# Performance work log

Hardware: AMD Instinct MI355X
Metric: run time of the kernel (lower is better)

The kernel has to match this reference:

```python
import jax, jax.numpy as jnp
import numpy as np

BN_EPS = 1e-5

def setup_inputs() -> dict:
    key = jax.random.key(0)
    ks = jax.random.split(key, 13)
    bs, ch, hei, wei = 4, 32, 32, 128  # n_features = wei = 128, ch = n_features//4
    nf = wei
    def p(k, shape, s=0.05):
        return jax.random.normal(k, shape, dtype=jnp.float32) * s
    return {
        "head": jax.random.normal(ks[0], (bs, ch, hei, wei), dtype=jnp.float32),
        "tail": jax.random.normal(ks[1], (bs, ch, hei, wei), dtype=jnp.float32),
        "R_q": p(ks[2], (nf, nf)), "R_k": p(ks[3], (nf, nf)),
        "R_v": p(ks[4], (nf, nf)), "R_W": p(ks[5], (nf, nf)),
        "F_q": p(ks[6], (nf, nf)), "F_k": p(ks[7], (nf, nf)),
        "F_v": p(ks[8], (nf, nf)), "F_W": p(ks[9], (nf, nf)),
        "conv_w": p(ks[10], (2, 2 * ch, 1, 1)),
        "conv_b": jnp.zeros((2,), jnp.float32),
        "bn_w": jnp.ones((2,), jnp.float32),
        "bn_b": jnp.zeros((2,), jnp.float32),
        "bn_mean": jnp.zeros((2,), jnp.float32),
        "bn_var": jnp.ones((2,), jnp.float32),
        "flag": 1,
    }

def _affinity(head, tail, conv_w, conv_b, bn_w, bn_b, bn_mean, bn_var):
    # 1x1 conv -> eval-mode BatchNorm2d -> ReLU -> softmax over channel dim
    x = jnp.concatenate([head, tail], axis=1)                       # [b,2c,h,w]
    a = jnp.einsum('bchw,oc->bohw', x, conv_w[:, :, 0, 0]) + conv_b[None, :, None, None]
    scale = (bn_w / jnp.sqrt(bn_var + BN_EPS))[None, :, None, None]
    a = (a - bn_mean[None, :, None, None]) * scale + bn_b[None, :, None, None]
    a = jax.nn.relu(a)
    return jax.nn.softmax(a, axis=1)                                # torch legacy dim=1 for 4D

def reference(head, tail, R_q, R_k, R_v, R_W, F_q, F_k, F_v, F_W,
              conv_w, conv_b, bn_w, bn_b, bn_mean, bn_var, flag):
    bs, ch, hei, wei = head.shape
    L = hei * wei
    ic = ch  # inter_channels == ch by construction
    aff = _affinity(head, tail, conv_w, conv_b, bn_w, bn_b, bn_mean, bn_var)
    if flag:
        alpha = aff[:, 0].reshape(bs, L, 1)                          # broadcast over last axis
        q = (head @ R_q).reshape(bs, ic, L).transpose(0, 2, 1)       # [b,L,ic]
        t_k = (tail @ F_k).reshape(bs, ic, L).transpose(0, 2, 1)     # [b,L,ic]
        t_v = (tail @ F_v).reshape(bs, ic, L)                        # [b,ic,L]
        f_t = t_k @ t_v                                              # [b,L,L]
        h_k = (head @ R_k).reshape(bs, ic, L).transpose(0, 2, 1)
        h_v = (head @ R_v).reshape(bs, ic, L)
        f_h = h_k @ h_v                                              # [b,L,L]
        att = jax.nn.softmax(alpha * f_t + f_h, axis=-1)
        y = (att @ q).transpose(0, 2, 1).reshape(bs, ic, hei, wei)
        return y @ R_W + head
    else:
        alpha = aff[:, 1].reshape(bs, L, 1)
        q = (tail @ F_q).reshape(bs, ic, L).transpose(0, 2, 1)
        h_k = (head @ R_k).reshape(bs, ic, L).transpose(0, 2, 1)
        h_v = (head @ R_v).reshape(bs, ic, L)
        f_h = h_k @ h_v
        t_k = (tail @ F_k).reshape(bs, ic, L).transpose(0, 2, 1)
        t_v = (tail @ F_v).reshape(bs, ic, L)
        f_t = t_k @ t_v
        att = jax.nn.softmax(alpha * f_h + f_t, axis=-1)
        y = (att @ q).transpose(0, 2, 1).reshape(bs, ic, hei, wei)
        return y @ F_W + tail
```

## Files before the change

kernel.cpp:

```cpp
#include <hip/hip_runtime.h>
#include <hip/hip_bf16.h>
#include <stdint.h>

typedef unsigned short u16;
typedef unsigned int u32;
typedef __attribute__((ext_vector_type(8))) short short8;
typedef __attribute__((ext_vector_type(4))) short short4_t;
typedef __attribute__((ext_vector_type(4))) float f32x4;
typedef __attribute__((ext_vector_type(16))) float f32x16;

#define MFMA16(A,B,C) __builtin_amdgcn_mfma_f32_16x16x32_bf16((A),(B),(C),0,0,0)
#define MFMA32(A,B,C) __builtin_amdgcn_mfma_f32_32x32x16_bf16((A),(B),(C),0,0,0)
#define L2E 1.4426950408889634f

__device__ __forceinline__ u16 f2bf(float f) {
  u32 x = __float_as_uint(f);
  u32 r = x + 0x7fffu + ((x >> 16) & 1u);
  return (u16)(r >> 16);
}
__device__ __forceinline__ float bf2f(short v) {
  return __uint_as_float((u32)(u16)v << 16);
}
__device__ __forceinline__ u32 pack_bf2(float a, float b) {
  __hip_bfloat162 h = __float22bfloat162_rn(make_float2(a, b));
  u32 u; __builtin_memcpy(&u, &h, 4); return u;
}
__device__ __forceinline__ short8 mk_frag(u32 w0, u32 w1, u32 w2, u32 w3) {
  union { u32 u[4]; short8 s; } cv;
  cv.u[0] = w0; cv.u[1] = w1; cv.u[2] = w2; cv.u[3] = w3;
  return cv.s;
}

#if __has_builtin(__builtin_amdgcn_permlane32_swap)
__device__ __forceinline__ float half_max(float x) {
  u32 xu = __float_as_uint(x);
  auto a = __builtin_amdgcn_permlane32_swap(xu, xu, false, false);
  return fmaxf(__uint_as_float(a[0]), __uint_as_float(a[1]));
}
__device__ __forceinline__ float half_sum(float x) {
  u32 xu = __float_as_uint(x);
  auto a = __builtin_amdgcn_permlane32_swap(xu, xu, false, false);
  return __uint_as_float(a[0]) + __uint_as_float(a[1]);
}
#else
__device__ __forceinline__ float half_max(float x) {
  return fmaxf(x, __shfl_xor(x, 32, 64));
}
__device__ __forceinline__ float half_sum(float x) {
  return x + __shfl_xor(x, 32, 64);
}
#endif

__global__ void kprep(const float* R_q, const float* R_k, const float* R_v,
                      const float* R_W, const float* F_q, const float* F_k,
                      const float* F_v, const float* F_W, const int* flagp,
                      u16* matT)
{
  int flag = *flagp;
  const float* S;
  int m = blockIdx.x;
  if (flag) {
    const float* s[6] = {R_q, R_k, R_v, F_k, F_v, R_W}; S = s[m];
  } else {
    const float* s[6] = {F_q, F_k, F_v, R_k, R_v, F_W}; S = s[m];
  }
  u16* dst = matT + m * 16384;
  int base = blockIdx.y * 2048;
  for (int idx = base + threadIdx.x; idx < base + 2048; idx += blockDim.x) {
    int k = idx >> 7, n = idx & 127;
    dst[n * 128 + k] = f2bf(S[idx]);
  }
}

__global__ __launch_bounds__(256) void kproj(const float* __restrict__ head,
    const float* __restrict__ tail, const u16* __restrict__ matT,
    const float* __restrict__ conv_w, const float* __restrict__ conv_b,
    const float* __restrict__ bn_w, const float* __restrict__ bn_b,
    const float* __restrict__ bn_mean, const float* __restrict__ bn_var,
    u16* __restrict__ qT, u16* __restrict__ KQ,
    u16* __restrict__ Vc, const int* __restrict__ flagp)
{
  __shared__ u16 lds_t[128][34];
  __shared__ float s_alpha[128];
  const int flag = *flagp;
  const float* X1 = flag ? head : tail;
  const float* X2 = flag ? tail : head;
  const int bh = blockIdx.x, g = blockIdx.y;
  const int b = bh >> 5, h = bh & 31;
  const float* src = (g < 3) ? X1 : X2;
  const u16* Bm = matT + g * 16384;
  const int tid = threadIdx.x, lane = tid & 63, wid = tid >> 6;
  const int lrow = lane & 15, lg = lane >> 4;
  const int rt = wid & 1, cbase = (wid >> 1) * 64;

  if (g == 3) {
    if (tid < 128) {
      int w = tid;
      const float* hp = head + ((size_t)b * 1024 + h) * 128 + w;
      const float* tp = tail + ((size_t)b * 1024 + h) * 128 + w;
      float a0 = 0.f, a1 = 0.f;
      for (int c = 0; c < 32; ++c) {
        float xh = hp[c * 4096];
        float xt = tp[c * 4096];
        a0 += xh * conv_w[c]      + xt * conv_w[32 + c];
        a1 += xh * conv_w[64 + c] + xt * conv_w[96 + c];
      }
      const float eps = 1e-5f;
      a0 += conv_b[0]; a1 += conv_b[1];
      a0 = (a0 - bn_mean[0]) * (bn_w[0] * rsqrtf(bn_var[0] + eps)) + bn_b[0];
      a1 = (a1 - bn_mean[1]) * (bn_w[1] * rsqrtf(bn_var[1] + eps)) + bn_b[1];
      a0 = fmaxf(a0, 0.f); a1 = fmaxf(a1, 0.f);
      float asel = flag ? a0 : a1, aoth = flag ? a1 : a0;
      s_alpha[w] = 1.f / (1.f + __expf(aoth - asel));
    }
    __syncthreads();
  }

  f32x4 acc[4] = {};
  const float* Arow = src + (((size_t)b * 32 + rt * 16 + lrow) * 32 + h) * 128;
  #pragma unroll
  for (int k0 = 0; k0 < 128; k0 += 32) {
    const float* ap = Arow + k0 + lg * 8;
    float4 f0 = *reinterpret_cast<const float4*>(ap);
    float4 f1 = *reinterpret_cast<const float4*>(ap + 4);
    short8 af = mk_frag(pack_bf2(f0.x, f0.y), pack_bf2(f0.z, f0.w),
                        pack_bf2(f1.x, f1.y), pack_bf2(f1.z, f1.w));
    #pragma unroll
    for (int cc = 0; cc < 4; ++cc) {
      short8 bf = *reinterpret_cast<const short8*>(
          Bm + (cbase + cc * 16 + lrow) * 128 + k0 + lg * 8);
      acc[cc] = MFMA16(af, bf, acc[cc]);
    }
  }
  #pragma unroll
  for (int cc = 0; cc < 4; ++cc) {
    int n = cbase + cc * 16 + lrow;
    float asc = (g == 1) ? L2E : 1.f;
    if (g == 3) asc = s_alpha[n] * L2E;
    #pragma unroll
    for (int rr = 0; rr < 4; ++rr) {
      int c = rt * 16 + lg * 4 + rr;
      lds_t[n][c] = f2bf(acc[cc][rr] * asc);
    }
  }
  __syncthreads();
  if (g == 0) {
    int c = tid >> 3, w0 = (tid & 7) * 16;
    int tw[8];
    #pragma unroll
    for (int i2 = 0; i2 < 8; ++i2)
      tw[i2] = (int)lds_t[w0 + 2 * i2][c] | ((int)lds_t[w0 + 2 * i2 + 1][c] << 16);
    int4* dst = reinterpret_cast<int4*>(qT + ((size_t)b * 32 + c) * 4096 + h * 128 + w0);
    dst[0] = make_int4(tw[0], tw[1], tw[2], tw[3]);
    dst[1] = make_int4(tw[4], tw[5], tw[6], tw[7]);
  } else if (tid < 128) {
    int w = tid;
    int tw[16];
    #pragma unroll
    for (int i2 = 0; i2 < 16; ++i2)
      tw[i2] = (int)lds_t[w][2 * i2] | ((int)lds_t[w][2 * i2 + 1] << 16);
    u16* base = (g == 2 || g == 4) ? Vc : KQ;
    int coff = (g >= 3) ? 32 : 0;
    int4* dst = reinterpret_cast<int4*>(base + ((size_t)b * 4096 + h * 128 + w) * 64 + coff);
    dst[0] = make_int4(tw[0],  tw[1],  tw[2],  tw[3]);
    dst[1] = make_int4(tw[4],  tw[5],  tw[6],  tw[7]);
    dst[2] = make_int4(tw[8],  tw[9],  tw[10], tw[11]);
    dst[3] = make_int4(tw[12], tw[13], tw[14], tw[15]);
  }
}

__global__ __launch_bounds__(256, 4) void kattn(const u16* __restrict__ qT,
    const u16* __restrict__ KQ, const u16* __restrict__ Vc,
    u16* __restrict__ pO, float* __restrict__ pm, float* __restrict__ pl)
{
  __shared__ __align__(16) char lds_v[2][8192];
  __shared__ __align__(16) char lds_q[2][4096];
  const int b = blockIdx.y;
  const int i0 = blockIdx.x * 128;
  const int sp = blockIdx.z;
  const int jbase = sp * 512;
  const int tid = threadIdx.x, lane = tid & 63, wid = tid >> 6;
  const int l31 = lane & 31, h = lane >> 5;
  const int iw = i0 + wid * 32;

  const u16* KQb = KQ + (size_t)b * 4096 * 64;
  const u16* Vb  = Vc + (size_t)b * 4096 * 64;
  const u16* qTb = qT + (size_t)b * 32 * 4096;

  short8 bkq[4];
  #pragma unroll
  for (int c = 0; c < 4; ++c)
    bkq[c] = *reinterpret_cast<const short8*>(
        KQb + (size_t)(iw + l31) * 64 + c * 16 + h * 8);

  const int sr = tid >> 3, sx = (tid & 7) * 16;
  const int pr0 = (sr & ~12) | ((sr & 4) << 1) | ((sr & 8) >> 1);

  #pragma unroll
  for (int q = 0; q < 2; ++q) {
    int r = sr + q * 32, gr = pr0 + q * 32;
    int4 v = *reinterpret_cast<const int4*>(
        reinterpret_cast<const char*>(Vb + (size_t)(jbase + gr) * 64) + sx);
    *reinterpret_cast<int4*>(lds_v[0] + r * 128 + (sx ^ ((r & 7) << 4))) = v;
  }
  {
    int4 qv = *reinterpret_cast<const int4*>(
        qTb + (size_t)sr * 4096 + jbase + (tid & 7) * 8);
    *reinterpret_cast<int4*>(lds_q[0] + sr * 128 + (sx ^ ((sr & 7) << 4))) = qv;
  }
  __syncthreads();

  float m_run = -1e30f, l_run = 0.f;
  f32x16 accO = {};
  int4 stgV[2], stgQ;

  for (int t = 0; t < 8; ++t) {
    const int buf = t & 1;
    if (t < 7) {
      const u16* Vn = Vb + (size_t)(jbase + (t + 1) * 64) * 64;
      #pragma unroll
      for (int q = 0; q < 2; ++q) {
        int gr = pr0 + q * 32;
        stgV[q] = *reinterpret_cast<const int4*>(
            reinterpret_cast<const char*>(Vn + (size_t)gr * 64) + sx);
      }
      stgQ = *reinterpret_cast<const int4*>(
          qTb + (size_t)sr * 4096 + jbase + (t + 1) * 64 + (tid & 7) * 8);
    }
    f32x16 st[2];
    st[0] = f32x16{}; st[1] = f32x16{};
    __builtin_amdgcn_s_setprio(1);
    #pragma unroll
    for (int jt = 0; jt < 2; ++jt) {
      int vr = jt * 32 + l31;
      #pragma unroll
      for (int c = 0; c < 4; ++c) {
        short8 av = *reinterpret_cast<const short8*>(
            lds_v[buf] + vr * 128 + ((c * 32 + h * 16) ^ ((vr & 7) << 4)));
        st[jt] = MFMA32(av, bkq[c], st[jt]);
      }
    }
    __builtin_amdgcn_s_setprio(0);
    short8 aq[4];
    #pragma unroll
    for (int cc = 0; cc < 4; ++cc)
      aq[cc] = *reinterpret_cast<const short8*>(
          lds_q[buf] + l31 * 128 + ((cc * 32 + h * 16) ^ ((l31 & 7) << 4)));
    float tm = -1e30f;
    #pragma unroll
    for (int jt = 0; jt < 2; ++jt)
      #pragma unroll
      for (int r = 0; r < 16; ++r) tm = fmaxf(tm, st[jt][r]);
    tm = half_max(tm);
    if (!__all((int)(tm <= m_run + 8.f))) {
      float m_new = fmaxf(m_run, tm);
      float scale = exp2f(m_run - m_new);
      l_run *= scale;
      #pragma unroll
      for (int r = 0; r < 16; ++r) accO[r] *= scale;
      m_run = m_new;
    }
    float ps = 0.f;
    #pragma unroll
    for (int jt = 0; jt < 2; ++jt)
      #pragma unroll
      for (int r = 0; r < 16; ++r) {
        float p = exp2f(st[jt][r] - m_run);
        st[jt][r] = p;
        ps += p;
      }
    l_run += half_sum(ps);

    __builtin_amdgcn_s_setprio(1);
    #pragma unroll
    for (int cc = 0; cc < 4; ++cc) {
      const int jt = cc >> 1, p8 = (cc & 1) * 8;
      short8 bp = mk_frag(pack_bf2(st[jt][p8 + 0], st[jt][p8 + 1]),
                          pack_bf2(st[jt][p8 + 2], st[jt][p8 + 3]),
                          pack_bf2(st[jt][p8 + 4], st[jt][p8 + 5]),
                          pack_bf2(st[jt][p8 + 6], st[jt][p8 + 7]));
      accO = MFMA32(aq[cc], bp, accO);
    }
    __builtin_amdgcn_s_setprio(0);

    if (t < 7) {
      #pragma unroll
      for (int q = 0; q < 2; ++q) {
        int r = sr + q * 32;
        *reinterpret_cast<int4*>(lds_v[buf ^ 1] + r * 128 + (sx ^ ((r & 7) << 4))) = stgV[q];
      }
      *reinterpret_cast<int4*>(lds_q[buf ^ 1] + sr * 128 + (sx ^ ((sr & 7) << 4))) = stgQ;
      __syncthreads();
    }
  }

  const int i = iw + l31;
  u16* pOb = pO + (size_t)((b * 8 + sp) * 32) * 4096;
  #pragma unroll
  for (int r = 0; r < 16; ++r) {
    int c = (r & 3) + 8 * (r >> 2) + 4 * h;
    pOb[(size_t)c * 4096 + i] = f2bf(accO[r]);
  }
  if (h == 0) {
    pm[(b * 8 + sp) * 4096 + i] = m_run;
    pl[(b * 8 + sp) * 4096 + i] = l_run;
  }
}

__global__ __launch_bounds__(256) void kout(const u16* __restrict__ pO,
    const float* __restrict__ pm, const float* __restrict__ pl,
    const u16* __restrict__ matT, const float* __restrict__ head,
    const float* __restrict__ tail, const int* __restrict__ flagp,
    float* __restrict__ out)
{
  __shared__ u16 ylds[32][136];
  const int flag = *flagp;
  const float* X1 = flag ? head : tail;
  const u16* Bm = matT + 5 * 16384;
  const int tid = threadIdx.x;
  const int b = blockIdx.x >> 5, c = blockIdx.x & 31;
  const int rbase = blockIdx.x * 32;
  const int ioff = tid * 16;

  #pragma unroll
  for (int iq = 0; iq < 4; ++iq) {
    float4 msp[8];
    #pragma unroll
    for (int sp = 0; sp < 8; ++sp)
      msp[sp] = *reinterpret_cast<const float4*>(
          pm + (size_t)((b * 8 + sp) * 4096) + ioff + iq * 4);
    float4 M4 = msp[0];
    #pragma unroll
    for (int sp = 1; sp < 8; ++sp) {
      M4.x = fmaxf(M4.x, msp[sp].x); M4.y = fmaxf(M4.y, msp[sp].y);
      M4.z = fmaxf(M4.z, msp[sp].z); M4.w = fmaxf(M4.w, msp[sp].w);
    }
    float4 L4 = {0.f, 0.f, 0.f, 0.f}, y4 = {0.f, 0.f, 0.f, 0.f};
    #pragma unroll
    for (int sp = 0; sp < 8; ++sp) {
      float4 w4;
      w4.x = exp2f(msp[sp].x - M4.x); w4.y = exp2f(msp[sp].y - M4.y);
      w4.z = exp2f(msp[sp].z - M4.z); w4.w = exp2f(msp[sp].w - M4.w);
      float4 l4 = *reinterpret_cast<const float4*>(
          pl + (size_t)((b * 8 + sp) * 4096) + ioff + iq * 4);
      L4.x += w4.x * l4.x; L4.y += w4.y * l4.y;
      L4.z += w4.z * l4.z; L4.w += w4.w * l4.w;
      short4_t o4 = *reinterpret_cast<const short4_t*>(
          pO + (size_t)(((b * 8 + sp) * 32 + c)) * 4096 + ioff + iq * 4);
      y4.x += w4.x * bf2f(o4[0]); y4.y += w4.y * bf2f(o4[1]);
      y4.z += w4.z * bf2f(o4[2]); y4.w += w4.w * bf2f(o4[3]);
    }
    y4.x /= L4.x; y4.y /= L4.y; y4.z /= L4.z; y4.w /= L4.w;
    uint2 pk2;
    pk2.x = pack_bf2(y4.x, y4.y);
    pk2.y = pack_bf2(y4.z, y4.w);
    *reinterpret_cast<uint2*>(&ylds[tid >> 3][(tid & 7) * 16 + iq * 4]) = pk2;
  }
  __syncthreads();

  const int lane = tid & 63, wid = tid >> 6;
  const int lrow = lane & 15, lg = lane >> 4;
  const int rg = (wid & 1) * 16, cg = (wid >> 1) * 64;
  f32x4 acc[4] = {};
  #pragma unroll
  for (int k0 = 0; k0 < 128; k0 += 32) {
    short8 af = *reinterpret_cast<const short8*>(&ylds[rg + lrow][k0 + lg * 8]);
    #pragma unroll
    for (int cc = 0; cc < 4; ++cc) {
      short8 bf = *reinterpret_cast<const short8*>(
          Bm + (size_t)(cg + cc * 16 + lrow) * 128 + k0 + lg * 8);
      acc[cc] = MFMA16(af, bf, acc[cc]);
    }
  }
  #pragma unroll
  for (int cc = 0; cc < 4; ++cc)
    #pragma unroll
    for (int rr = 0; rr < 4; ++rr) {
      int row = rbase + rg + lg * 4 + rr;
      int col = cg + cc * 16 + lrow;
      size_t idx = (size_t)row * 128 + col;
      out[idx] = acc[cc][rr] + X1[idx];
    }
}

extern "C" void kernel_launch(void* const* d_in, const int* in_sizes, int n_in,
                              void* d_out, int out_size, void* d_ws, size_t ws_size,
                              hipStream_t stream)
{
  const float* head    = (const float*)d_in[0];
  const float* tail    = (const float*)d_in[1];
  const float* R_q     = (const float*)d_in[2];
  const float* R_k     = (const float*)d_in[3];
  const float* R_v     = (const float*)d_in[4];
  const float* R_W     = (const float*)d_in[5];
  const float* F_q     = (const float*)d_in[6];
  const float* F_k     = (const float*)d_in[7];
  const float* F_v     = (const float*)d_in[8];
  const float* F_W     = (const float*)d_in[9];
  const float* conv_w  = (const float*)d_in[10];
  const float* conv_b  = (const float*)d_in[11];
  const float* bn_w    = (const float*)d_in[12];
  const float* bn_b    = (const float*)d_in[13];
  const float* bn_mean = (const float*)d_in[14];
  const float* bn_var  = (const float*)d_in[15];
  const int*   flagp   = (const int*)d_in[16];
  float* out = (float*)d_out;

  char* ws = (char*)d_ws;
  u16*   matT = (u16*)(ws);
  u16*   qT   = (u16*)(ws + 262144);
  u16*   KQ   = (u16*)(ws + 1310720);
  u16*   Vc   = (u16*)(ws + 3407872);
  u16*   pO   = (u16*)(ws + 6553600);
  float* pm   = (float*)(ws + 14942208);
  float* pl   = (float*)(ws + 15466496);

  kprep <<<dim3(6, 8), 256, 0, stream>>>(R_q, R_k, R_v, R_W, F_q, F_k, F_v, F_W, flagp, matT);
  kproj <<<dim3(128, 5), 256, 0, stream>>>(head, tail, matT, conv_w, conv_b,
                                           bn_w, bn_b, bn_mean, bn_var,
                                           qT, KQ, Vc, flagp);
  kattn <<<dim3(32, 4, 8), 256, 0, stream>>>(qT, KQ, Vc, pO, pm, pl);
  kout  <<<128, 256, 0, stream>>>(pO, pm, pl, matT, head, tail, flagp, out);
}
```

Measured before the change: 64.12 us.

## Fuse weight transpose/bf16 conversion into projection and output kernels via LDS

Removes the separate kprep launch that wrote transposed bf16 weight matrices to global workspace. Each block of kproj and kout now loads its fp32 weight matrix, converts it to bf16 and transposes it into an XOR-swizzled 32KB LDS buffer, then reads MFMA B fragments from LDS. This saves one kernel launch and a global round trip, but every block redoes the transpose (640 blocks in kproj, 128 in kout). The added LDS use may also lower occupancy.

Measured after the change: 62.97 us. No clear change (-1.8%).

```diff
diff --git a/kernel.cpp b/kernel.cpp
--- a/kernel.cpp
+++ b/kernel.cpp
@@ -51,35 +51,39 @@
 }
 #endif
 
-__global__ void kprep(const float* R_q, const float* R_k, const float* R_v,
-                      const float* R_W, const float* F_q, const float* F_k,
-                      const float* F_v, const float* F_W, const int* flagp,
-                      u16* matT)
+__device__ __forceinline__ void transpose_to_lds(const float* __restrict__ Sg,
+                                                 char* btc, int tid)
 {
-  int flag = *flagp;
-  const float* S;
-  int m = blockIdx.x;
-  if (flag) {
-    const float* s[6] = {R_q, R_k, R_v, F_k, F_v, R_W}; S = s[m];
-  } else {
-    const float* s[6] = {F_q, F_k, F_v, R_k, R_v, F_W}; S = s[m];
-  }
-  u16* dst = matT + m * 16384;
-  int base = blockIdx.y * 2048;
-  for (int idx = base + threadIdx.x; idx < base + 2048; idx += blockDim.x) {
-    int k = idx >> 7, n = idx & 127;
-    dst[n * 128 + k] = f2bf(S[idx]);
+  const int kr = (tid >> 2) * 2;
+  const int nc = (tid & 3) * 32;
+  const float* r0 = Sg + kr * 128 + nc;
+  const float* r1 = r0 + 128;
+  #pragma unroll
+  for (int j4 = 0; j4 < 8; ++j4) {
+    float4 a = *reinterpret_cast<const float4*>(r0 + j4 * 4);
+    float4 b = *reinterpret_cast<const float4*>(r1 + j4 * 4);
+    #pragma unroll
+    for (int e = 0; e < 4; ++e) {
+      int n = nc + j4 * 4 + e;
+      float av = (&a.x)[e], bv = (&b.x)[e];
+      *reinterpret_cast<u32*>(btc + ((n * 256 + kr * 2) ^ ((n & 7) << 4))) =
+          pack_bf2(av, bv);
+    }
   }
 }
 
 __global__ __launch_bounds__(256) void kproj(const float* __restrict__ head,
-    const float* __restrict__ tail, const u16* __restrict__ matT,
+    const float* __restrict__ tail,
+    const float* __restrict__ R_q, const float* __restrict__ R_k,
+    const float* __restrict__ R_v, const float* __restrict__ F_q,
+    const float* __restrict__ F_k, const float* __restrict__ F_v,
     const float* __restrict__ conv_w, const float* __restrict__ conv_b,
     const float* __restrict__ bn_w, const float* __restrict__ bn_b,
     const float* __restrict__ bn_mean, const float* __restrict__ bn_var,
     u16* __restrict__ qT, u16* __restrict__ KQ,
     u16* __restrict__ Vc, const int* __restrict__ flagp)
 {
+  __shared__ __align__(16) char bt[32768];
   __shared__ u16 lds_t[128][34];
   __shared__ float s_alpha[128];
   const int flag = *flagp;
@@ -88,10 +92,15 @@
   const int bh = blockIdx.x, g = blockIdx.y;
   const int b = bh >> 5, h = bh & 31;
   const float* src = (g < 3) ? X1 : X2;
-  const u16* Bm = matT + g * 16384;
   const int tid = threadIdx.x, lane = tid & 63, wid = tid >> 6;
   const int lrow = lane & 15, lg = lane >> 4;
   const int rt = wid & 1, cbase = (wid >> 1) * 64;
+
+  {
+    const float* s1[5] = {R_q, R_k, R_v, F_k, F_v};
+    const float* s0[5] = {F_q, F_k, F_v, R_k, R_v};
+    transpose_to_lds(flag ? s1[g] : s0[g], bt, tid);
+  }
 
   if (g == 3) {
     if (tid < 128) {
@@ -113,8 +122,8 @@
       float asel = flag ? a0 : a1, aoth = flag ? a1 : a0;
       s_alpha[w] = 1.f / (1.f + __expf(aoth - asel));
     }
-    __syncthreads();
-  }
+  }
+  __syncthreads();
 
   f32x4 acc[4] = {};
   const float* Arow = src + (((size_t)b * 32 + rt * 16 + lrow) * 32 + h) * 128;
@@ -127,8 +136,9 @@
                         pack_bf2(f1.x, f1.y), pack_bf2(f1.z, f1.w));
     #pragma unroll
     for (int cc = 0; cc < 4; ++cc) {
+      int n = cbase + cc * 16 + lrow;
       short8 bf = *reinterpret_cast<const short8*>(
-          Bm + (cbase + cc * 16 + lrow) * 128 + k0 + lg * 8);
+          bt + ((n * 256 + k0 * 2 + lg * 16) ^ ((n & 7) << 4)));
       acc[cc] = MFMA16(af, bf, acc[cc]);
     }
   }
@@ -309,18 +319,20 @@
 
 __global__ __launch_bounds__(256) void kout(const u16* __restrict__ pO,
     const float* __restrict__ pm, const float* __restrict__ pl,
-    const u16* __restrict__ matT, const float* __restrict__ head,
-    const float* __restrict__ tail, const int* __restrict__ flagp,
-    float* __restrict__ out)
+    const float* __restrict__ R_W, const float* __restrict__ F_W,
+    const float* __restrict__ head, const float* __restrict__ tail,
+    const int* __restrict__ flagp, float* __restrict__ out)
 {
+  __shared__ __align__(16) char btW[32768];
   __shared__ u16 ylds[32][136];
   const int flag = *flagp;
   const float* X1 = flag ? head : tail;
-  const u16* Bm = matT + 5 * 16384;
   const int tid = threadIdx.x;
   const int b = blockIdx.x >> 5, c = blockIdx.x & 31;
   const int rbase = blockIdx.x * 32;
   const int ioff = tid * 16;
+
+  transpose_to_lds(flag ? R_W : F_W, btW, tid);
 
   #pragma unroll
   for (int iq = 0; iq < 4; ++iq) {
@@ -367,8 +379,9 @@
     short8 af = *reinterpret_cast<const short8*>(&ylds[rg + lrow][k0 + lg * 8]);
     #pragma unroll
     for (int cc = 0; cc < 4; ++cc) {
+      int n = cg + cc * 16 + lrow;
       short8 bf = *reinterpret_cast<const short8*>(
-          Bm + (size_t)(cg + cc * 16 + lrow) * 128 + k0 + lg * 8);
+          btW + ((n * 256 + k0 * 2 + lg * 16) ^ ((n & 7) << 4)));
       acc[cc] = MFMA16(af, bf, acc[cc]);
     }
   }
@@ -407,7 +420,6 @@
   float* out = (float*)d_out;
 
   char* ws = (char*)d_ws;
-  u16*   matT = (u16*)(ws);
   u16*   qT   = (u16*)(ws + 262144);
   u16*   KQ   = (u16*)(ws + 1310720);
   u16*   Vc   = (u16*)(ws + 3407872);
@@ -415,10 +427,10 @@
   float* pm   = (float*)(ws + 14942208);
   float* pl   = (float*)(ws + 15466496);
 
-  kprep <<<dim3(6, 8), 256, 0, stream>>>(R_q, R_k, R_v, R_W, F_q, F_k, F_v, F_W, flagp, matT);
-  kproj <<<dim3(128, 5), 256, 0, stream>>>(head, tail, matT, conv_w, conv_b,
+  kproj <<<dim3(128, 5), 256, 0, stream>>>(head, tail, R_q, R_k, R_v,
+                                           F_q, F_k, F_v, conv_w, conv_b,
                                            bn_w, bn_b, bn_mean, bn_var,
                                            qT, KQ, Vc, flagp);
   kattn <<<dim3(32, 4, 8), 256, 0, stream>>>(qT, KQ, Vc, pO, pm, pl);
-  kout  <<<128, 256, 0, stream>>>(pO, pm, pl, matT, head, tail, flagp, out);
-}
+  kout  <<<128, 256, 0, stream>>>(pO, pm, pl, R_W, F_W, head, tail, flagp, out);
+}
```
